# Kernel optimization log

Measured on AMD Instinct MI355X. Metric: run time of the kernel, lower is better.

The kernel has to match this reference:

```python
import jax, jax.numpy as jnp
import numpy as np

EMBED_DIM = 128
MAX_LEN = 256.0
LN_EPS = 1e-5


def sinusoidal_pe(x, embed_dim, embed_size):
    # x: [..., ] float; returns [..., embed_dim]
    inv_freq = 1.0 / embed_size ** (2.0 * jnp.arange(embed_dim // 2, dtype=jnp.float32) / embed_dim)
    angles = x[..., None] * jnp.float32(np.pi) * inv_freq
    return jnp.concatenate([jnp.sin(angles), jnp.cos(angles)], axis=-1)


def setup_inputs() -> dict:
    key = jax.random.key(0)
    ks = jax.random.split(key, 20)
    B, N, A = 4, 256, 4
    input_nf, hidden_nf, output_nf = 128, 256, 128
    edge_in = 2 * input_nf + EMBED_DIM + 3  # 387

    def lin(k, fan_in, fan_out):
        bound = 1.0 / np.sqrt(fan_in)
        kw, kb = jax.random.split(k)
        W = jax.random.uniform(kw, (fan_in, fan_out), jnp.float32, -bound, bound)
        b = jax.random.uniform(kb, (fan_out,), jnp.float32, -bound, bound)
        return W, b

    We1, be1 = lin(ks[0], edge_in, hidden_nf)
    We2, be2 = lin(ks[1], hidden_nf, hidden_nf)
    Wn1, bn1 = lin(ks[2], input_nf + hidden_nf, hidden_nf)
    Wn2, bn2 = lin(ks[3], hidden_nf, output_nf)
    Wc1, bc1 = lin(ks[4], hidden_nf, hidden_nf)
    Wc2, bc2 = lin(ks[5], hidden_nf, 1)

    coords = jax.random.normal(ks[6], (B, N, A, 3), jnp.float32)
    node_features = jax.random.normal(ks[7], (B, N, input_nf), jnp.float32)
    atom_mask = jnp.ones((B, N, A), jnp.float32)
    residue_indices = jnp.sort(jax.random.randint(ks[8], (B, N), 0, 256), axis=-1).astype(jnp.int32)

    return dict(coords=coords, node_features=node_features, atom_mask=atom_mask,
                residue_indices=residue_indices,
                We1=We1, be1=be1, We2=We2, be2=be2,
                Wn1=Wn1, bn1=bn1, Wn2=Wn2, bn2=bn2,
                gamma=jnp.ones((output_nf,), jnp.float32), beta=jnp.zeros((output_nf,), jnp.float32),
                Wc1=Wc1, bc1=bc1, Wc2=Wc2, bc2=bc2)


def reference(coords, node_features, atom_mask, residue_indices,
              We1, be1, We2, be2, Wn1, bn1, Wn2, bn2, gamma, beta,
              Wc1, bc1, Wc2, bc2):
    B, N, A, _ = coords.shape
    # relative residue offsets -> sinusoidal PE: [B,N,N,embed_dim]
    rel = (residue_indices[:, :, None] - residue_indices[:, None, :]).astype(jnp.float32)
    rel_enc = sinusoidal_pe(rel, EMBED_DIM, MAX_LEN)
    # directional vectors: mean over atoms of pairwise coord diffs -> [B,N,N,3]
    dirs = (coords[:, :, None, :, :] - coords[:, None, :, :, :]).mean(axis=3)
    # pairwise edge features [B,N,N,2*F+E+3]
    fi = jnp.broadcast_to(node_features[:, :, None, :], (B, N, N, node_features.shape[-1]))
    fj = jnp.broadcast_to(node_features[:, None, :, :], (B, N, N, node_features.shape[-1]))
    edge_feat = jnp.concatenate([fi, fj, rel_enc, dirs], axis=-1)
    msg = jax.nn.silu(jax.nn.silu(edge_feat @ We1 + be1) @ We2 + be2)  # [B,N,N,H]
    agg = msg.sum(axis=2)  # [B,N,H]
    h = jnp.concatenate([node_features, agg], axis=-1)
    h = jax.nn.silu(h @ Wn1 + bn1) @ Wn2 + bn2  # [B,N,output_nf]
    mu = h.mean(axis=-1, keepdims=True)
    var = ((h - mu) ** 2).mean(axis=-1, keepdims=True)
    h = (h - mu) / jnp.sqrt(var + LN_EPS) * gamma + beta
    cu = jax.nn.silu(msg @ Wc1 + bc1) @ Wc2 + bc2  # [B,N,N,1]
    coord_updates = (cu * dirs).sum(axis=2)  # [B,N,3]
    updated_coords = coords + coord_updates[:, :, None, :] * atom_mask[..., None]
    return updated_coords, h
```

## Files before the change

kernel.cpp:

```cpp
#include <hip/hip_runtime.h>

typedef unsigned short u16;
typedef __attribute__((ext_vector_type(8))) _Float16 hfrag8;
typedef __attribute__((ext_vector_type(4))) float f32x4;

__device__ __forceinline__ float bu2f(u16 u) { return __uint_as_float(((unsigned)u) << 16); }
__device__ __forceinline__ u16 f2bu(float f) {
    unsigned x = __float_as_uint(f);
    return (u16)((x + 0x7fffu + ((x >> 16) & 1u)) >> 16);
}
__device__ __forceinline__ u16 f2hu(float f) {
    _Float16 h = (_Float16)f;
    return __builtin_bit_cast(u16, h);
}
__device__ __forceinline__ float ldf(const void* p, int i, bool f32) {
    return f32 ? ((const float*)p)[i] : bu2f(((const u16*)p)[i]);
}
__device__ __forceinline__ float siluf(float x) {
    return x * __builtin_amdgcn_rcpf(1.0f + __expf(-x));
}
__device__ __forceinline__ unsigned pkh(float a, float b) {
    return __builtin_bit_cast(unsigned, __builtin_amdgcn_cvt_pkrtz(a, b));
}
__device__ __forceinline__ bool detect_f32(const void* nf, int t) {
    const u16* p = (const u16*)nf;
    u16 v = p[(t & 255) * 2];
    int e = (v >> 7) & 0xFF;
    int ext = (e >= 140 || e == 0) ? 1 : 0;
    return __syncthreads_count(ext) > 32;
}

__global__ __launch_bounds__(256) void prep_kernel(
    const void* __restrict__ coords, const void* __restrict__ nf,
    const void* __restrict__ We1, const void* __restrict__ be1,
    const void* __restrict__ We2, const void* __restrict__ Wc1,
    float* __restrict__ cbar, float* __restrict__ pi2, float* __restrict__ qd,
    float* __restrict__ Ttab, u16* __restrict__ We2X, u16* __restrict__ Wc1X)
{
    const int t = threadIdx.x;
    const bool f32 = detect_f32(nf, t);
    const int blk = blockIdx.x;

    __shared__ float nf_l[4][128];
    __shared__ float ctmp[4][12];
    __shared__ float cb_l[4][3];
    __shared__ float pe[128];
    __shared__ u16 tile[32][33];

    if (blk < 256) {
        const int row0 = blk * 4;
        for (int idx = t; idx < 512; idx += 256) {
            int r = idx >> 7, k = idx & 127;
            nf_l[r][k] = ldf(nf, (row0 + r) * 128 + k, f32);
        }
        if (t < 48) ctmp[t / 12][t % 12] = ldf(coords, row0 * 12 + t, f32);
        __syncthreads();
        if (t < 12) {
            int r = t / 3, x = t % 3;
            float m = 0.25f * (ctmp[r][x] + ctmp[r][3 + x] + ctmp[r][6 + x] + ctmp[r][9 + x]);
            cb_l[r][x] = m;
            cbar[(row0 + r) * 3 + x] = m;
        }
        __syncthreads();
        const int n = t;
        float accP[4] = {0.f, 0.f, 0.f, 0.f}, accQ[4] = {0.f, 0.f, 0.f, 0.f};
        for (int k = 0; k < 128; k++) {
            float w1 = ldf(We1, k * 256 + n, f32);
            float w2 = ldf(We1, (128 + k) * 256 + n, f32);
#pragma unroll
            for (int r = 0; r < 4; r++) {
                accP[r] += nf_l[r][k] * w1;
                accQ[r] += nf_l[r][k] * w2;
            }
        }
        float wx = ldf(We1, 384 * 256 + n, f32);
        float wy = ldf(We1, 385 * 256 + n, f32);
        float wz = ldf(We1, 386 * 256 + n, f32);
        float b1 = ldf(be1, n, f32);
#pragma unroll
        for (int r = 0; r < 4; r++) {
            float d = cb_l[r][0] * wx + cb_l[r][1] * wy + cb_l[r][2] * wz;
            pi2[(row0 + r) * 256 + n] = accP[r] + d + b1;
            qd[(row0 + r) * 256 + n]  = accQ[r] - d;
        }
    } else if (blk < 767) {
        const float d = (float)(blk - 511);
        if (t < 64) {
            float ang = d * 3.14159265358979323846f * exp2f(-(float)t * 0.125f);
            pe[t] = sinf(ang);
            pe[64 + t] = cosf(ang);
        }
        __syncthreads();
        float acc = 0.f;
        for (int k = 0; k < 128; k++) acc += pe[k] * ldf(We1, (256 + k) * 256 + t, f32);
        Ttab[(blk - 256) * 256 + t] = acc;
    } else {
        int tbf = blk - 767;
        int mat = tbf >> 6;
        int tb = tbf & 63;
        int bx = tb & 7, by = tb >> 3;
        const void* src = mat ? Wc1 : We2;
        u16* dst = mat ? Wc1X : We2X;
        int tx = threadIdx.x & 31, ty = threadIdx.x >> 5;
#pragma unroll
        for (int p = 0; p < 4; p++) {
            int r = by * 32 + ty + p * 8;
            tile[ty + p * 8][tx] = f2hu(ldf(src, r * 256 + bx * 32 + tx, f32));
        }
        __syncthreads();
#pragma unroll
        for (int p = 0; p < 4; p++) {
            int n = bx * 32 + ty + p * 8;
            dst[((n >> 4) * 8 + by) * 512 + (n & 15) * 32 + tx] = tile[tx][ty + p * 8];
        }
    }
}

__global__ __launch_bounds__(256, 1)
void edge_kernel(
    const int* __restrict__ resid,
    const float* __restrict__ pi2, const float* __restrict__ qd,
    const float* __restrict__ Ttab, const float* __restrict__ cbar,
    const u16* __restrict__ We2X, const u16* __restrict__ Wc1X,
    const void* __restrict__ be2, const void* __restrict__ bc1,
    const void* __restrict__ Wc2, const void* __restrict__ bc2,
    const void* __restrict__ nf,
    float* __restrict__ agg_out, float* __restrict__ cupd_out)
{
    const int t = threadIdx.x;
    const bool f32 = detect_f32(nf, t);
    const int node = blockIdx.x;
    const int b = node >> 8;
    const int lane = t & 63, w = t >> 6;
    const int c = lane & 15, q = lane >> 4;

    __shared__ __align__(16) u16 U[128][280];
    __shared__ int relidx[256];
    __shared__ float fin[4][4];

    relidx[t] = resid[node] - resid[(b << 8) + t] + 255;
    const float bc2q = 0.25f * ldf(bc2, 0, f32);

    float4 be2v[4], bc1v[4], wc2v[4];
#pragma unroll
    for (int n = 0; n < 4; n++) {
        const int base = w * 64 + n * 16 + q * 4;
        be2v[n] = make_float4(ldf(be2, base, f32), ldf(be2, base + 1, f32),
                              ldf(be2, base + 2, f32), ldf(be2, base + 3, f32));
        bc1v[n] = make_float4(ldf(bc1, base, f32), ldf(bc1, base + 1, f32),
                              ldf(bc1, base + 2, f32), ldf(bc1, base + 3, f32));
        wc2v[n] = make_float4(ldf(Wc2, base, f32), ldf(Wc2, base + 1, f32),
                              ldf(Wc2, base + 2, f32), ldf(Wc2, base + 3, f32));
    }

    const int kp = lane << 2;
    const float4 pv = *(const float4*)(pi2 + node * 256 + kp);

    float aggv[4][4] = {{0.f}};
    float s0 = 0.f, s1 = 0.f, s2 = 0.f, s3 = 0.f;

    const f32x4 zf = {0.f, 0.f, 0.f, 0.f};
    __syncthreads();

    for (int jc = 0; jc < 2; jc++) {
        const int j0 = jc << 7;
        {
            const float* qbase = qd + ((b << 8) + j0) * 256 + kp;
            const int r0 = w * 32;
#pragma unroll 4
            for (int jj = 0; jj < 32; jj++) {
                const int j = r0 + jj;
                const float4 qv = *(const float4*)(qbase + j * 256);
                const float4 tv = *(const float4*)(Ttab + relidx[j0 + j] * 256 + kp);
                uint2 pk;
                pk.x = pkh(siluf(pv.x + qv.x + tv.x), siluf(pv.y + qv.y + tv.y));
                pk.y = pkh(siluf(pv.z + qv.z + tv.z), siluf(pv.w + qv.w + tv.w));
                *(uint2*)&U[j][kp] = pk;
            }
        }
        __syncthreads();

        f32x4 acc[8][4];
#pragma unroll
        for (int m = 0; m < 8; m++)
#pragma unroll
            for (int n = 0; n < 4; n++) acc[m][n] = zf;
#pragma unroll 2
        for (int ks = 0; ks < 8; ks++) {
            const int kb = ks * 32 + q * 8;
            hfrag8 wf[4];
#pragma unroll
            for (int n = 0; n < 4; n++)
                wf[n] = *(const hfrag8*)(We2X + ((w * 4 + n) * 8 + ks) * 512 + c * 32 + q * 8);
            hfrag8 hm[8];
#pragma unroll
            for (int m = 0; m < 8; m++)
                hm[m] = *(const hfrag8*)&U[m * 16 + c][kb];
#pragma unroll
            for (int m = 0; m < 8; m++)
#pragma unroll
                for (int n = 0; n < 4; n++)
                    acc[m][n] = __builtin_amdgcn_mfma_f32_16x16x32_f16(wf[n], hm[m], acc[m][n], 0, 0, 0);
        }
        __syncthreads();

#pragma unroll
        for (int m = 0; m < 8; m++) {
            u16* mrow = &U[m * 16 + c][w * 64 + q * 4];
#pragma unroll
            for (int n = 0; n < 4; n++) {
                float sa = siluf(acc[m][n][0] + be2v[n].x);
                float sb = siluf(acc[m][n][1] + be2v[n].y);
                float sc_ = siluf(acc[m][n][2] + be2v[n].z);
                float sd = siluf(acc[m][n][3] + be2v[n].w);
                aggv[n][0] += sa; aggv[n][1] += sb;
                aggv[n][2] += sc_; aggv[n][3] += sd;
                uint2 pk;
                pk.x = pkh(sa, sb);
                pk.y = pkh(sc_, sd);
                *(uint2*)(mrow + n * 16) = pk;
            }
        }
        __syncthreads();

#pragma unroll
        for (int m = 0; m < 8; m++)
#pragma unroll
            for (int n = 0; n < 4; n++) acc[m][n] = zf;
#pragma unroll 2
        for (int ks = 0; ks < 8; ks++) {
            const int kb = ks * 32 + q * 8;
            hfrag8 wf[4];
#pragma unroll
            for (int n = 0; n < 4; n++)
                wf[n] = *(const hfrag8*)(Wc1X + ((w * 4 + n) * 8 + ks) * 512 + c * 32 + q * 8);
            hfrag8 mm[8];
#pragma unroll
            for (int m = 0; m < 8; m++)
                mm[m] = *(const hfrag8*)&U[m * 16 + c][kb];
#pragma unroll
            for (int m = 0; m < 8; m++)
#pragma unroll
                for (int n = 0; n < 4; n++)
                    acc[m][n] = __builtin_amdgcn_mfma_f32_16x16x32_f16(wf[n], mm[m], acc[m][n], 0, 0, 0);
        }
        __syncthreads();

#pragma unroll
        for (int m = 0; m < 8; m++) {
            float dv = 0.f;
#pragma unroll
            for (int n = 0; n < 4; n++) {
                dv += siluf(acc[m][n][0] + bc1v[n].x) * wc2v[n].x;
                dv += siluf(acc[m][n][1] + bc1v[n].y) * wc2v[n].y;
                dv += siluf(acc[m][n][2] + bc1v[n].z) * wc2v[n].z;
                dv += siluf(acc[m][n][3] + bc1v[n].w) * wc2v[n].w;
            }
            dv += __shfl_xor(dv, 16);
            dv += __shfl_xor(dv, 32);
            if (q == 0) {
                const float vb = dv + bc2q;
                const float* cp = cbar + ((b << 8) + j0 + m * 16 + c) * 3;
                s0 += vb;
                s1 += vb * cp[0];
                s2 += vb * cp[1];
                s3 += vb * cp[2];
            }
        }
    }

#pragma unroll
    for (int n = 0; n < 4; n++)
#pragma unroll
        for (int r = 0; r < 4; r++) {
            float v = aggv[n][r];
            v += __shfl_xor(v, 1);
            v += __shfl_xor(v, 2);
            v += __shfl_xor(v, 4);
            v += __shfl_xor(v, 8);
            aggv[n][r] = v;
        }
    if (c == 0) {
#pragma unroll
        for (int n = 0; n < 4; n++) {
            float4 o = make_float4(aggv[n][0], aggv[n][1], aggv[n][2], aggv[n][3]);
            *(float4*)(agg_out + node * 256 + w * 64 + n * 16 + q * 4) = o;
        }
    }

#pragma unroll
    for (int d = 1; d < 16; d <<= 1) {
        s0 += __shfl_xor(s0, d);
        s1 += __shfl_xor(s1, d);
        s2 += __shfl_xor(s2, d);
        s3 += __shfl_xor(s3, d);
    }
    if (lane == 0) { fin[w][0] = s0; fin[w][1] = s1; fin[w][2] = s2; fin[w][3] = s3; }
    __syncthreads();
    if (t == 0) {
        float S0 = fin[0][0] + fin[1][0] + fin[2][0] + fin[3][0];
        float S1 = fin[0][1] + fin[1][1] + fin[2][1] + fin[3][1];
        float S2 = fin[0][2] + fin[1][2] + fin[2][2] + fin[3][2];
        float S3 = fin[0][3] + fin[1][3] + fin[2][3] + fin[3][3];
        const float cx = cbar[node * 3 + 0], cy = cbar[node * 3 + 1], cz = cbar[node * 3 + 2];
        cupd_out[node * 3 + 0] = S0 * cx - S1;
        cupd_out[node * 3 + 1] = S0 * cy - S2;
        cupd_out[node * 3 + 2] = S0 * cz - S3;
    }
}

__global__ __launch_bounds__(256) void out_kernel(
    const void* __restrict__ nf, const float* __restrict__ agg,
    const void* __restrict__ Wn1, const void* __restrict__ bn1,
    const void* __restrict__ Wn2, const void* __restrict__ bn2,
    const void* __restrict__ gamma, const void* __restrict__ beta,
    const void* __restrict__ coords, const void* __restrict__ mask,
    const float* __restrict__ cupd, void* __restrict__ d_out)
{
    const int t = threadIdx.x;
    const bool f32 = detect_f32(nf, t);

    if (blockIdx.x >= 128) {
        int idx = (blockIdx.x - 128) * 256 + t;
        if (idx < 4 * 256 * 4 * 3) {
            int x = idx % 3;
            int a = (idx / 3) & 3;
            int node = idx / 12;
            float v = ldf(coords, idx, f32) + cupd[node * 3 + x] * ldf(mask, node * 4 + a, f32);
            if (f32) ((float*)d_out)[idx] = v;
            else     ((u16*)d_out)[idx] = f2bu(v);
        }
        return;
    }

    const int row0 = blockIdx.x * 8;
    __shared__ float x_l[8][384];
    __shared__ float hs[8][256];
    __shared__ float ho[8][128];
    for (int idx = t; idx < 8 * 384; idx += 256) {
        int r = idx / 384, k = idx % 384;
        x_l[r][k] = (k < 128) ? ldf(nf, (row0 + r) * 128 + k, f32)
                              : agg[(row0 + r) * 256 + (k - 128)];
    }
    __syncthreads();
    {
        float a1[8] = {0.f, 0.f, 0.f, 0.f, 0.f, 0.f, 0.f, 0.f};
        for (int k = 0; k < 384; k++) {
            float wv = ldf(Wn1, k * 256 + t, f32);
#pragma unroll
            for (int r = 0; r < 8; r++) a1[r] += x_l[r][k] * wv;
        }
        float b1 = ldf(bn1, t, f32);
#pragma unroll
        for (int r = 0; r < 8; r++) hs[r][t] = siluf(a1[r] + b1);
    }
    __syncthreads();
    {
        int cc = t & 127, rg = (t >> 7) * 4;
        float a2[4] = {0.f, 0.f, 0.f, 0.f};
        for (int k = 0; k < 256; k++) {
            float wv = ldf(Wn2, k * 128 + cc, f32);
#pragma unroll
            for (int r = 0; r < 4; r++) a2[r] += hs[rg + r][k] * wv;
        }
        float b2 = ldf(bn2, cc, f32);
#pragma unroll
        for (int r = 0; r < 4; r++) ho[rg + r][cc] = a2[r] + b2;
    }
    __syncthreads();
    {
        int row = t >> 5, s = t & 31;
        float sm = 0.f, sq = 0.f;
#pragma unroll
        for (int u = 0; u < 4; u++) {
            float v = ho[row][s + 32 * u];
            sm += v; sq += v * v;
        }
#pragma unroll
        for (int d = 1; d < 32; d <<= 1) {
            sm += __shfl_xor(sm, d);
            sq += __shfl_xor(sq, d);
        }
        float mu = sm * (1.f / 128.f);
        float var = sq * (1.f / 128.f) - mu * mu;
        float inv = rsqrtf(var + 1e-5f);
#pragma unroll
        for (int u = 0; u < 4; u++) {
            int cc = s + 32 * u;
            float y = (ho[row][cc] - mu) * inv;
            float outv = y * ldf(gamma, cc, f32) + ldf(beta, cc, f32);
            int oi = 12288 + (row0 + row) * 128 + cc;
            if (f32) ((float*)d_out)[oi] = outv;
            else     ((u16*)d_out)[oi] = f2bu(outv);
        }
    }
}

extern "C" void kernel_launch(void* const* d_in, const int* in_sizes, int n_in,
                              void* d_out, int out_size, void* d_ws, size_t ws_size,
                              hipStream_t stream)
{
    const void* coords = d_in[0];
    const void* nf     = d_in[1];
    const void* mask   = d_in[2];
    const int* resid   = (const int*)d_in[3];
    const void* We1 = d_in[4];
    const void* be1 = d_in[5];
    const void* We2 = d_in[6];
    const void* be2 = d_in[7];
    const void* Wn1 = d_in[8];
    const void* bn1 = d_in[9];
    const void* Wn2 = d_in[10];
    const void* bn2 = d_in[11];
    const void* gamma = d_in[12];
    const void* beta  = d_in[13];
    const void* Wc1 = d_in[14];
    const void* bc1 = d_in[15];
    const void* Wc2 = d_in[16];
    const void* bc2 = d_in[17];

    float* f   = (float*)d_ws + 16;
    float* cbar = f;
    float* pi2  = cbar + 3072;
    float* qd   = pi2 + 262144;
    float* Ttab = qd + 262144;
    float* agg  = Ttab + 130816;
    float* cupd = agg + 262144;
    u16* We2X = (u16*)(cupd + 3072);
    u16* Wc1X = We2X + 65536;

    hipLaunchKernelGGL(prep_kernel, dim3(895), dim3(256), 0, stream,
                       coords, nf, We1, be1, We2, Wc1, cbar, pi2, qd, Ttab, We2X, Wc1X);
    hipLaunchKernelGGL(edge_kernel, dim3(1024), dim3(256), 0, stream,
                       resid, pi2, qd, Ttab, cbar, We2X, Wc1X, be2, bc1, Wc2, bc2, nf, agg, cupd);
    hipLaunchKernelGGL(out_kernel, dim3(176), dim3(256), 0, stream,
                       nf, agg, Wn1, bn1, Wn2, bn2, gamma, beta, coords, mask, cupd, d_out);
}
```

Before: 372.8 us.

## Split edge kernel work across eight waves per block instead of four

Doubles the edge kernel block to 512 threads, so each of eight waves owns 32 output columns instead of 64 and builds 16 rows of the first-layer activation tile instead of 32. Per-wave accumulator count is halved, which cuts register pressure and gives each CU more waves to hide MFMA and LDS latency. The bc2 share and the final reduction are adjusted for eight waves, and detect_f32 is guarded so only the first 256 threads read. The cost is more barrier participants and B-fragment LDS reads that are now repeated by twice as many waves.

```diff
diff --git a/kernel.cpp b/kernel.cpp
--- a/kernel.cpp
+++ b/kernel.cpp
@@ -24,9 +24,12 @@
 }
 __device__ __forceinline__ bool detect_f32(const void* nf, int t) {
     const u16* p = (const u16*)nf;
-    u16 v = p[(t & 255) * 2];
-    int e = (v >> 7) & 0xFF;
-    int ext = (e >= 140 || e == 0) ? 1 : 0;
+    int ext = 0;
+    if (t < 256) {
+        u16 v = p[t * 2];
+        int e = (v >> 7) & 0xFF;
+        ext = (e >= 140 || e == 0) ? 1 : 0;
+    }
     return __syncthreads_count(ext) > 32;
 }
 
@@ -116,7 +119,7 @@
     }
 }
 
-__global__ __launch_bounds__(256, 1)
+__global__ __launch_bounds__(512, 1)
 void edge_kernel(
     const int* __restrict__ resid,
     const float* __restrict__ pi2, const float* __restrict__ qd,
@@ -136,27 +139,27 @@
 
     __shared__ __align__(16) u16 U[128][280];
     __shared__ int relidx[256];
-    __shared__ float fin[4][4];
-
-    relidx[t] = resid[node] - resid[(b << 8) + t] + 255;
-    const float bc2q = 0.25f * ldf(bc2, 0, f32);
-
-    float4 be2v[4], bc1v[4], wc2v[4];
-#pragma unroll
-    for (int n = 0; n < 4; n++) {
-        const int base = w * 64 + n * 16 + q * 4;
-        be2v[n] = make_float4(ldf(be2, base, f32), ldf(be2, base + 1, f32),
-                              ldf(be2, base + 2, f32), ldf(be2, base + 3, f32));
-        bc1v[n] = make_float4(ldf(bc1, base, f32), ldf(bc1, base + 1, f32),
-                              ldf(bc1, base + 2, f32), ldf(bc1, base + 3, f32));
-        wc2v[n] = make_float4(ldf(Wc2, base, f32), ldf(Wc2, base + 1, f32),
-                              ldf(Wc2, base + 2, f32), ldf(Wc2, base + 3, f32));
+    __shared__ float fin[8][4];
+
+    if (t < 256) relidx[t] = resid[node] - resid[(b << 8) + t] + 255;
+    const float bc2q = 0.125f * ldf(bc2, 0, f32);
+
+    float4 be2v[2], bc1v[2], wc2v[2];
+#pragma unroll
+    for (int nn = 0; nn < 2; nn++) {
+        const int base = w * 32 + nn * 16 + q * 4;
+        be2v[nn] = make_float4(ldf(be2, base, f32), ldf(be2, base + 1, f32),
+                               ldf(be2, base + 2, f32), ldf(be2, base + 3, f32));
+        bc1v[nn] = make_float4(ldf(bc1, base, f32), ldf(bc1, base + 1, f32),
+                               ldf(bc1, base + 2, f32), ldf(bc1, base + 3, f32));
+        wc2v[nn] = make_float4(ldf(Wc2, base, f32), ldf(Wc2, base + 1, f32),
+                               ldf(Wc2, base + 2, f32), ldf(Wc2, base + 3, f32));
     }
 
     const int kp = lane << 2;
     const float4 pv = *(const float4*)(pi2 + node * 256 + kp);
 
-    float aggv[4][4] = {{0.f}};
+    float aggv[2][4] = {{0.f}};
     float s0 = 0.f, s1 = 0.f, s2 = 0.f, s3 = 0.f;
 
     const f32x4 zf = {0.f, 0.f, 0.f, 0.f};
@@ -166,9 +169,9 @@
         const int j0 = jc << 7;
         {
             const float* qbase = qd + ((b << 8) + j0) * 256 + kp;
-            const int r0 = w * 32;
+            const int r0 = w * 16;
 #pragma unroll 4
-            for (int jj = 0; jj < 32; jj++) {
+            for (int jj = 0; jj < 16; jj++) {
                 const int j = r0 + jj;
                 const float4 qv = *(const float4*)(qbase + j * 256);
                 const float4 tv = *(const float4*)(Ttab + relidx[j0 + j] * 256 + kp);
@@ -180,18 +183,18 @@
         }
         __syncthreads();
 
-        f32x4 acc[8][4];
+        f32x4 acc[8][2];
 #pragma unroll
         for (int m = 0; m < 8; m++)
 #pragma unroll
-            for (int n = 0; n < 4; n++) acc[m][n] = zf;
+            for (int nn = 0; nn < 2; nn++) acc[m][nn] = zf;
 #pragma unroll 2
         for (int ks = 0; ks < 8; ks++) {
             const int kb = ks * 32 + q * 8;
-            hfrag8 wf[4];
-#pragma unroll
-            for (int n = 0; n < 4; n++)
-                wf[n] = *(const hfrag8*)(We2X + ((w * 4 + n) * 8 + ks) * 512 + c * 32 + q * 8);
+            hfrag8 wf[2];
+#pragma unroll
+            for (int nn = 0; nn < 2; nn++)
+                wf[nn] = *(const hfrag8*)(We2X + ((w * 2 + nn) * 8 + ks) * 512 + c * 32 + q * 8);
             hfrag8 hm[8];
 #pragma unroll
             for (int m = 0; m < 8; m++)
@@ -199,26 +202,26 @@
 #pragma unroll
             for (int m = 0; m < 8; m++)
 #pragma unroll
-                for (int n = 0; n < 4; n++)
-                    acc[m][n] = __builtin_amdgcn_mfma_f32_16x16x32_f16(wf[n], hm[m], acc[m][n], 0, 0, 0);
+                for (int nn = 0; nn < 2; nn++)
+                    acc[m][nn] = __builtin_amdgcn_mfma_f32_16x16x32_f16(wf[nn], hm[m], acc[m][nn], 0, 0, 0);
         }
         __syncthreads();
 
 #pragma unroll
         for (int m = 0; m < 8; m++) {
-            u16* mrow = &U[m * 16 + c][w * 64 + q * 4];
-#pragma unroll
-            for (int n = 0; n < 4; n++) {
-                float sa = siluf(acc[m][n][0] + be2v[n].x);
-                float sb = siluf(acc[m][n][1] + be2v[n].y);
-                float sc_ = siluf(acc[m][n][2] + be2v[n].z);
-                float sd = siluf(acc[m][n][3] + be2v[n].w);
-                aggv[n][0] += sa; aggv[n][1] += sb;
-                aggv[n][2] += sc_; aggv[n][3] += sd;
+            u16* mrow = &U[m * 16 + c][w * 32 + q * 4];
+#pragma unroll
+            for (int nn = 0; nn < 2; nn++) {
+                float sa = siluf(acc[m][nn][0] + be2v[nn].x);
+                float sb = siluf(acc[m][nn][1] + be2v[nn].y);
+                float sc_ = siluf(acc[m][nn][2] + be2v[nn].z);
+                float sd = siluf(acc[m][nn][3] + be2v[nn].w);
+                aggv[nn][0] += sa; aggv[nn][1] += sb;
+                aggv[nn][2] += sc_; aggv[nn][3] += sd;
                 uint2 pk;
                 pk.x = pkh(sa, sb);
                 pk.y = pkh(sc_, sd);
-                *(uint2*)(mrow + n * 16) = pk;
+                *(uint2*)(mrow + nn * 16) = pk;
             }
         }
         __syncthreads();
@@ -226,14 +229,14 @@
 #pragma unroll
         for (int m = 0; m < 8; m++)
 #pragma unroll
-            for (int n = 0; n < 4; n++) acc[m][n] = zf;
+            for (int nn = 0; nn < 2; nn++) acc[m][nn] = zf;
 #pragma unroll 2
         for (int ks = 0; ks < 8; ks++) {
             const int kb = ks * 32 + q * 8;
-            hfrag8 wf[4];
-#pragma unroll
-            for (int n = 0; n < 4; n++)
-                wf[n] = *(const hfrag8*)(Wc1X + ((w * 4 + n) * 8 + ks) * 512 + c * 32 + q * 8);
+            hfrag8 wf[2];
+#pragma unroll
+            for (int nn = 0; nn < 2; nn++)
+                wf[nn] = *(const hfrag8*)(Wc1X + ((w * 2 + nn) * 8 + ks) * 512 + c * 32 + q * 8);
             hfrag8 mm[8];
 #pragma unroll
             for (int m = 0; m < 8; m++)
@@ -241,8 +244,8 @@
 #pragma unroll
             for (int m = 0; m < 8; m++)
 #pragma unroll
-                for (int n = 0; n < 4; n++)
-                    acc[m][n] = __builtin_amdgcn_mfma_f32_16x16x32_f16(wf[n], mm[m], acc[m][n], 0, 0, 0);
+                for (int nn = 0; nn < 2; nn++)
+                    acc[m][nn] = __builtin_amdgcn_mfma_f32_16x16x32_f16(wf[nn], mm[m], acc[m][nn], 0, 0, 0);
         }
         __syncthreads();
 
@@ -250,11 +253,11 @@
         for (int m = 0; m < 8; m++) {
             float dv = 0.f;
 #pragma unroll
-            for (int n = 0; n < 4; n++) {
-                dv += siluf(acc[m][n][0] + bc1v[n].x) * wc2v[n].x;
-                dv += siluf(acc[m][n][1] + bc1v[n].y) * wc2v[n].y;
-                dv += siluf(acc[m][n][2] + bc1v[n].z) * wc2v[n].z;
-                dv += siluf(acc[m][n][3] + bc1v[n].w) * wc2v[n].w;
+            for (int nn = 0; nn < 2; nn++) {
+                dv += siluf(acc[m][nn][0] + bc1v[nn].x) * wc2v[nn].x;
+                dv += siluf(acc[m][nn][1] + bc1v[nn].y) * wc2v[nn].y;
+                dv += siluf(acc[m][nn][2] + bc1v[nn].z) * wc2v[nn].z;
+                dv += siluf(acc[m][nn][3] + bc1v[nn].w) * wc2v[nn].w;
             }
             dv += __shfl_xor(dv, 16);
             dv += __shfl_xor(dv, 32);
@@ -270,21 +273,21 @@
     }
 
 #pragma unroll
-    for (int n = 0; n < 4; n++)
+    for (int nn = 0; nn < 2; nn++)
 #pragma unroll
         for (int r = 0; r < 4; r++) {
-            float v = aggv[n][r];
+            float v = aggv[nn][r];
             v += __shfl_xor(v, 1);
             v += __shfl_xor(v, 2);
             v += __shfl_xor(v, 4);
             v += __shfl_xor(v, 8);
-            aggv[n][r] = v;
+            aggv[nn][r] = v;
         }
     if (c == 0) {
 #pragma unroll
-        for (int n = 0; n < 4; n++) {
-            float4 o = make_float4(aggv[n][0], aggv[n][1], aggv[n][2], aggv[n][3]);
-            *(float4*)(agg_out + node * 256 + w * 64 + n * 16 + q * 4) = o;
+        for (int nn = 0; nn < 2; nn++) {
+            float4 o = make_float4(aggv[nn][0], aggv[nn][1], aggv[nn][2], aggv[nn][3]);
+            *(float4*)(agg_out + node * 256 + w * 32 + nn * 16 + q * 4) = o;
         }
     }
 
@@ -298,10 +301,11 @@
     if (lane == 0) { fin[w][0] = s0; fin[w][1] = s1; fin[w][2] = s2; fin[w][3] = s3; }
     __syncthreads();
     if (t == 0) {
-        float S0 = fin[0][0] + fin[1][0] + fin[2][0] + fin[3][0];
-        float S1 = fin[0][1] + fin[1][1] + fin[2][1] + fin[3][1];
-        float S2 = fin[0][2] + fin[1][2] + fin[2][2] + fin[3][2];
-        float S3 = fin[0][3] + fin[1][3] + fin[2][3] + fin[3][3];
+        float S0 = 0.f, S1 = 0.f, S2 = 0.f, S3 = 0.f;
+#pragma unroll
+        for (int u = 0; u < 8; u++) {
+            S0 += fin[u][0]; S1 += fin[u][1]; S2 += fin[u][2]; S3 += fin[u][3];
+        }
         const float cx = cbar[node * 3 + 0], cy = cbar[node * 3 + 1], cz = cbar[node * 3 + 2];
         cupd_out[node * 3 + 0] = S0 * cx - S1;
         cupd_out[node * 3 + 1] = S0 * cy - S2;
@@ -431,7 +435,7 @@
 
     hipLaunchKernelGGL(prep_kernel, dim3(895), dim3(256), 0, stream,
                        coords, nf, We1, be1, We2, Wc1, cbar, pi2, qd, Ttab, We2X, Wc1X);
-    hipLaunchKernelGGL(edge_kernel, dim3(1024), dim3(256), 0, stream,
+    hipLaunchKernelGGL(edge_kernel, dim3(1024), dim3(512), 0, stream,
                        resid, pi2, qd, Ttab, cbar, We2X, Wc1X, be2, bc1, Wc2, bc2, nf, agg, cupd);
     hipLaunchKernelGGL(out_kernel, dim3(176), dim3(256), 0, stream,
                        nf, agg, Wn1, bn1, Wn2, bn2, gamma, beta, coords, mask, cupd, d_out);
```

Result: faster. 318.0 us (-14.7%).
